# Kernel tuning notes

Measured on AMD Instinct MI355X. Metric: run time of the kernel, lower is better.

The kernel has to match this reference:

```python
import jax, jax.numpy as jnp
import numpy as np

N, L, D = 4096, 16, 768        # nodes, max name tokens, gpt2 embed dim
NH_NAME = 4                    # name-encoder attention heads
H, NH, NL, C = 1024, 8, 4, 16  # hidden, encoder heads, encoder layers, classes
XF = 256                       # raw node feature dim; feat_dim = XF + D = 1024
VOCAB = 50257


def _ln(x, g, b, eps=1e-5):
    m = jnp.mean(x, axis=-1, keepdims=True)
    v = jnp.var(x, axis=-1, keepdims=True)
    return (x - m) * jax.lax.rsqrt(v + eps) * g + b


def _mha(x, in_w, in_b, out_w, out_b, nh, key_mask=None):
    # x: [B, S, E]; in_w: [3E, E] (torch nn.MultiheadAttention packed qkv)
    B, S, E = x.shape
    dh = E // nh
    qkv = x @ in_w.T + in_b
    q, k, v = jnp.split(qkv, 3, axis=-1)
    q = q.reshape(B, S, nh, dh)
    k = k.reshape(B, S, nh, dh)
    v = v.reshape(B, S, nh, dh)
    scores = jnp.einsum('bqhd,bkhd->bhqk', q, k) / jnp.sqrt(jnp.asarray(dh, x.dtype))
    if key_mask is not None:
        scores = jnp.where(key_mask[:, None, None, :], scores, jnp.asarray(-1e9, x.dtype))
    a = jax.nn.softmax(scores, axis=-1)
    o = jnp.einsum('bhqk,bkhd->bqhd', a, v).reshape(B, S, E)
    return o @ out_w.T + out_b


def setup_inputs() -> dict:
    key = jax.random.key(0)
    ks = jax.random.split(key, 16)
    s = 0.02
    r = lambda i, shape: jax.random.normal(ks[i], shape, jnp.float32) * s
    return {
        'name_tokens': jax.random.randint(ks[0], (N, L), 0, VOCAB),
        'name_lens': jax.random.randint(ks[1], (N,), 1, L + 1),
        'x_feats': jax.random.normal(ks[2], (N, XF), jnp.float32),
        'wte': r(3, (VOCAB, D)),
        'mha_in_w': r(4, (3 * D, D)), 'mha_in_b': jnp.zeros((3 * D,), jnp.float32),
        'mha_out_w': r(5, (D, D)), 'mha_out_b': jnp.zeros((D,), jnp.float32),
        'bott_w': r(6, (H, XF + D)), 'bott_b': jnp.zeros((H,), jnp.float32),
        'enc_in_w': r(7, (NL, 3 * H, H)), 'enc_in_b': jnp.zeros((NL, 3 * H), jnp.float32),
        'enc_out_w': r(8, (NL, H, H)), 'enc_out_b': jnp.zeros((NL, H), jnp.float32),
        'enc_ln1_g': jnp.ones((NL, H), jnp.float32), 'enc_ln1_b': jnp.zeros((NL, H), jnp.float32),
        'enc_ln2_g': jnp.ones((NL, H), jnp.float32), 'enc_ln2_b': jnp.zeros((NL, H), jnp.float32),
        'enc_ff1_w': r(9, (NL, 2 * H, H)), 'enc_ff1_b': jnp.zeros((NL, 2 * H), jnp.float32),
        'enc_ff2_w': r(10, (NL, H, 2 * H)), 'enc_ff2_b': jnp.zeros((NL, H), jnp.float32),
        'cls_w': r(11, (C, H)), 'cls_b': jnp.zeros((C,), jnp.float32),
    }


def reference(name_tokens, name_lens, x_feats, wte,
              mha_in_w, mha_in_b, mha_out_w, mha_out_b,
              bott_w, bott_b,
              enc_in_w, enc_in_b, enc_out_w, enc_out_b,
              enc_ln1_g, enc_ln1_b, enc_ln2_g, enc_ln2_b,
              enc_ff1_w, enc_ff1_b, enc_ff2_w, enc_ff2_b,
              cls_w, cls_b):
    # --- GraphNameEncoder: batched over all N ragged name sequences ---
    mask = jnp.arange(L)[None, :] < name_lens[:, None]          # [N, L] valid-token mask
    emb = wte[name_tokens]                                      # [N, L, D]
    attn = _mha(emb, mha_in_w, mha_in_b, mha_out_w, mha_out_b, NH_NAME, key_mask=mask)
    name_emb = jnp.sum(jnp.where(mask[:, :, None], attn, 0.0), axis=1)  # [N, D]
    x = jnp.concatenate([x_feats, name_emb], axis=-1)           # [N, XF + D]
    # --- bottleneck ---
    x = x @ bott_w.T + bott_b                                   # [N, H]
    # --- TransformerEncoder on seq_len=1 (x.unsqueeze(1)), post-norm, relu ---
    h = x[:, None, :]                                           # [N, 1, H]
    for l in range(NL):
        a = _mha(h, enc_in_w[l], enc_in_b[l], enc_out_w[l], enc_out_b[l], NH)
        h = _ln(h + a, enc_ln1_g[l], enc_ln1_b[l])
        f = jax.nn.relu(h @ enc_ff1_w[l].T + enc_ff1_b[l]) @ enc_ff2_w[l].T + enc_ff2_b[l]
        h = _ln(h + f, enc_ln2_g[l], enc_ln2_b[l])
    out = h @ cls_w.T + cls_b                                   # [N, 1, C]
    return out[:, 0, :]                                         # squeeze -> [N, C]
```

## Files before the change

kernel.cpp:

```cpp
#include <hip/hip_runtime.h>

typedef unsigned short bf16_t;
typedef __attribute__((ext_vector_type(8))) __bf16 bf16x8;
typedef __attribute__((ext_vector_type(4))) float f32x4;

__device__ __forceinline__ float bf2f(unsigned v) { return __uint_as_float(v << 16); }
__device__ __forceinline__ bf16_t f2bf(float f) {
  unsigned u = __float_as_uint(f);
  return (bf16_t)((u + 0x7fffu + ((u >> 16) & 1u)) >> 16);
}
__device__ __forceinline__ unsigned pack2(float a, float b) {
  return (unsigned)f2bf(a) | ((unsigned)f2bf(b) << 16);
}

__global__ __launch_bounds__(256) void scan_lens(const int* __restrict__ lens,
                                                 int* __restrict__ offs,
                                                 int* __restrict__ Mact) {
  __shared__ int wsum[4];
  const int t = threadIdx.x;
  int v[16]; int s = 0;
#pragma unroll
  for (int i = 0; i < 16; i++) { v[i] = lens[t * 16 + i]; s += v[i]; }
  const int lane = t & 63, w = t >> 6;
  int x = s;
#pragma unroll
  for (int o = 1; o < 64; o <<= 1) {
    int y = __shfl_up(x, o);
    if (lane >= o) x += y;
  }
  if (lane == 63) wsum[w] = x;
  __syncthreads();
  int base = 0;
  for (int i = 0; i < w; i++) base += wsum[i];
  int run = base + x - s;
#pragma unroll
  for (int i = 0; i < 16; i++) { offs[t * 16 + i] = run; run += v[i]; }
  if (t == 255) Mact[0] = run;
}

__global__ void cvt_f32_bf16(const float* __restrict__ src, bf16_t* __restrict__ dst, long n4) {
  long i = (long)blockIdx.x * blockDim.x + threadIdx.x;
  if (i >= n4) return;
  float4 v = ((const float4*)src)[i];
  ((uint2*)dst)[i] = make_uint2(pack2(v.x, v.y), pack2(v.z, v.w));
}

__global__ void cvt_encv(const float* __restrict__ src, bf16_t* __restrict__ dst, long n4) {
  long i = (long)blockIdx.x * blockDim.x + threadIdx.x;
  if (i >= n4) return;
  const long per = (1024L * 1024L) / 4;
  long l = i / per, r = i % per;
  const float* s = src + l * 3 * 1024 * 1024 + 2 * 1024 * 1024 + r * 4;
  float4 v = *(const float4*)s;
  ((uint2*)dst)[i] = make_uint2(pack2(v.x, v.y), pack2(v.z, v.w));
}

__global__ void gather_emb_c(const int* __restrict__ tok, const int* __restrict__ lens,
                             const int* __restrict__ offs, const float* __restrict__ wte,
                             bf16_t* __restrict__ emb) {
  long i = (long)blockIdx.x * blockDim.x + threadIdx.x;
  if (i >= 65536L * 192L) return;
  long nl = i / 192; int cg = (int)(i % 192);
  int n = (int)(nl >> 4), l = (int)(nl & 15);
  if (l >= lens[n]) return;
  long ro = (long)offs[n] + l;
  int t = tok[nl];
  float4 v = *(const float4*)(wte + (long)t * 768 + cg * 4);
  ((uint2*)emb)[ro * 192 + cg] = make_uint2(pack2(v.x, v.y), pack2(v.z, v.w));
}

__global__ void xfeat_lenf(const float* __restrict__ xf, const int* __restrict__ lens,
                           bf16_t* __restrict__ x, float* __restrict__ lenf) {
  long i = (long)blockIdx.x * blockDim.x + threadIdx.x;
  if (i < 4096) lenf[i] = (float)lens[i];
  if (i >= 4096L * 64L) return;
  int row = (int)(i >> 6); int c4 = (int)(i & 63) * 4;
  float4 v = *(const float4*)(xf + (long)row * 256 + c4);
  *(uint2*)(x + (long)row * 1024 + c4) = make_uint2(pack2(v.x, v.y), pack2(v.z, v.w));
}

#define BM 128
#define BN 128
#define BK 32

__device__ __forceinline__ void async16(const void* g, void* l) {
  __builtin_amdgcn_global_load_lds((const __attribute__((address_space(1))) void*)g,
                                   (__attribute__((address_space(3))) void*)l, 16, 0, 0);
}

__global__ __launch_bounds__(256, 2) void gemm_bt(
    const bf16_t* __restrict__ A, const bf16_t* __restrict__ W,
    const float* __restrict__ bias, bf16_t* __restrict__ C,
    int K, int ldc, const int* __restrict__ Mp) {
  const int m0 = blockIdx.y * BM;
  if (m0 >= *Mp) return;
  __shared__ __attribute__((aligned(16))) bf16_t As[BM * BK];
  __shared__ __attribute__((aligned(16))) bf16_t Bs[BN * BK];
  const int t = threadIdx.x;
  const int n0 = blockIdx.x * BN;
  const int lane = t & 63;
  const int wr = t >> 7;
  const int wc = (t >> 6) & 1;
  const int quad = lane >> 4;
  const int r16 = lane & 15;

  f32x4 acc[4][4] = {};

  const int c0 = t, c1 = t + 256;
  const int row0 = c0 >> 2, kp0 = (c0 & 3) << 3;
  const int row1 = c1 >> 2, kp1 = (c1 & 3) << 3;
  bf16_t* lA0 = As + (size_t)(c0 & ~63) * 8;
  bf16_t* lA1 = As + (size_t)(c1 & ~63) * 8;
  bf16_t* lB0 = Bs + (size_t)(c0 & ~63) * 8;
  bf16_t* lB1 = Bs + (size_t)(c1 & ~63) * 8;
  const bf16_t* Ab = A + (size_t)m0 * K;
  const bf16_t* Wb = W + (size_t)n0 * K;

  for (int k0 = 0; k0 < K; k0 += BK) {
    __syncthreads();
    async16(Ab + (size_t)row0 * K + k0 + kp0, lA0);
    async16(Ab + (size_t)row1 * K + k0 + kp1, lA1);
    async16(Wb + (size_t)row0 * K + k0 + kp0, lB0);
    async16(Wb + (size_t)row1 * K + k0 + kp1, lB1);
    __syncthreads();
    bf16x8 af[4], bfr[4];
#pragma unroll
    for (int i = 0; i < 4; i++) {
      af[i]  = *(const bf16x8*)(As + (wr * 64 + i * 16 + r16) * BK + quad * 8);
      bfr[i] = *(const bf16x8*)(Bs + (wc * 64 + i * 16 + r16) * BK + quad * 8);
    }
#pragma unroll
    for (int i = 0; i < 4; i++)
#pragma unroll
      for (int j = 0; j < 4; j++)
        acc[i][j] = __builtin_amdgcn_mfma_f32_16x16x32_bf16(af[i], bfr[j], acc[i][j], 0, 0, 0);
  }

  const int colb = n0 + wc * 64;
  const int rowb = m0 + wr * 64;
#pragma unroll
  for (int j = 0; j < 4; j++) {
    int col = colb + j * 16 + r16;
    float bv = bias ? bias[col] : 0.0f;
#pragma unroll
    for (int i = 0; i < 4; i++) {
      int rbase = rowb + i * 16 + quad * 4;
#pragma unroll
      for (int r = 0; r < 4; r++) {
        int row = rbase + r;
        C[(size_t)row * ldc + col] = f2bf(acc[i][j][r] + bv);
      }
    }
  }
}

template <bool RELU>
__global__ __launch_bounds__(256, 4) void gemm64(
    const bf16_t* __restrict__ A, const bf16_t* __restrict__ W,
    const float* __restrict__ bias, const float* __restrict__ rowscale,
    bf16_t* __restrict__ C, int K, int ldc) {
  __shared__ __attribute__((aligned(16))) bf16_t As[64 * 64];
  __shared__ __attribute__((aligned(16))) bf16_t Bs[64 * 64];
  const int t = threadIdx.x;
  const int m0 = blockIdx.y * 64, n0 = blockIdx.x * 64;
  const int lane = t & 63, wr = t >> 7, wc = (t >> 6) & 1;
  const int quad = lane >> 4, r16 = lane & 15;
  f32x4 acc[2][2] = {};
  const int c0 = t, c1 = t + 256;
  const int row0 = c0 >> 3, kp0 = (((c0 & 7) ^ (row0 & 7)) << 3);
  const int row1 = c1 >> 3, kp1 = (((c1 & 7) ^ (row1 & 7)) << 3);
  bf16_t* lA0 = As + (size_t)(c0 & ~63) * 8;
  bf16_t* lA1 = As + (size_t)(c1 & ~63) * 8;
  bf16_t* lB0 = Bs + (size_t)(c0 & ~63) * 8;
  bf16_t* lB1 = Bs + (size_t)(c1 & ~63) * 8;
  const bf16_t* Ab = A + (size_t)m0 * K;
  const bf16_t* Wb = W + (size_t)n0 * K;

  for (int k0 = 0; k0 < K; k0 += 64) {
    __syncthreads();
    async16(Ab + (size_t)row0 * K + k0 + kp0, lA0);
    async16(Ab + (size_t)row1 * K + k0 + kp1, lA1);
    async16(Wb + (size_t)row0 * K + k0 + kp0, lB0);
    async16(Wb + (size_t)row1 * K + k0 + kp1, lB1);
    __syncthreads();
#pragma unroll
    for (int kk8 = 0; kk8 < 8; kk8 += 4) {
      bf16x8 af[2], bfr[2];
#pragma unroll
      for (int i = 0; i < 2; i++) {
        int Ra = wr * 32 + i * 16 + r16;
        af[i] = *(const bf16x8*)(As + Ra * 64 + (((kk8 + quad) ^ (Ra & 7)) << 3));
        int Rb = wc * 32 + i * 16 + r16;
        bfr[i] = *(const bf16x8*)(Bs + Rb * 64 + (((kk8 + quad) ^ (Rb & 7)) << 3));
      }
#pragma unroll
      for (int i = 0; i < 2; i++)
#pragma unroll
        for (int j = 0; j < 2; j++)
          acc[i][j] = __builtin_amdgcn_mfma_f32_16x16x32_bf16(af[i], bfr[j], acc[i][j], 0, 0, 0);
    }
  }

  const int colb = n0 + wc * 32, rowb = m0 + wr * 32;
#pragma unroll
  for (int j = 0; j < 2; j++) {
    int col = colb + j * 16 + r16;
    float bv = bias ? bias[col] : 0.0f;
#pragma unroll
    for (int i = 0; i < 2; i++) {
      int rbase = rowb + i * 16 + quad * 4;
#pragma unroll
      for (int r = 0; r < 4; r++) {
        int row = rbase + r;
        float sc = rowscale ? rowscale[row] : 1.0f;
        float v = acc[i][j][r] + bv * sc;
        if (RELU) v = fmaxf(v, 0.0f);
        C[(size_t)row * ldc + col] = f2bf(v);
      }
    }
  }
}

__global__ __launch_bounds__(64) void attn_name(const bf16_t* __restrict__ qkv,
                                                const int* __restrict__ lens,
                                                const int* __restrict__ offs,
                                                bf16_t* __restrict__ s) {
  const int n = blockIdx.x, h = blockIdx.y;
  const int lane = threadIdx.x;
  __shared__ unsigned short qs[16][208];
  __shared__ unsigned short ks[16][208];
  __shared__ unsigned short vs[16][208];
  __shared__ float ps[16][16];
  __shared__ float wj[16];
  const int len = lens[n];
  const bf16_t* base = qkv + (size_t)offs[n] * 2304 + h * 192;
  for (int g = lane; g < len * 48; g += 64) {
    int row = g / 48, c4 = (g % 48) * 4;
    const bf16_t* p = base + (size_t)row * 2304 + c4;
    uint2 a;
    a = *(const uint2*)p;
    *(unsigned*)&qs[row][c4] = a.x; *(unsigned*)&qs[row][c4 + 2] = a.y;
    a = *(const uint2*)(p + 768);
    *(unsigned*)&ks[row][c4] = a.x; *(unsigned*)&ks[row][c4 + 2] = a.y;
    a = *(const uint2*)(p + 1536);
    *(unsigned*)&vs[row][c4] = a.x; *(unsigned*)&vs[row][c4 + 2] = a.y;
  }
  __syncthreads();
  {
    const int l = lane >> 2, j0 = (lane & 3) * 4;
    float s0 = 0, s1 = 0, s2 = 0, s3 = 0;
    for (int d = 0; d < 192; d++) {
      float q = bf2f(qs[l][d]);
      s0 += q * bf2f(ks[j0 + 0][d]);
      s1 += q * bf2f(ks[j0 + 1][d]);
      s2 += q * bf2f(ks[j0 + 2][d]);
      s3 += q * bf2f(ks[j0 + 3][d]);
    }
    const float sc = 0.07216878f;
    ps[l][j0 + 0] = s0 * sc; ps[l][j0 + 1] = s1 * sc;
    ps[l][j0 + 2] = s2 * sc; ps[l][j0 + 3] = s3 * sc;
  }
  __syncthreads();
  if (lane < 16) {
    float m = -1e30f;
    for (int j = 0; j < len; j++) m = fmaxf(m, ps[lane][j]);
    float sum = 0.f;
    for (int j = 0; j < len; j++) sum += __expf(ps[lane][j] - m);
    float inv = 1.0f / sum;
    for (int j = 0; j < 16; j++) ps[lane][j] = (j < len) ? __expf(ps[lane][j] - m) * inv : 0.0f;
  }
  __syncthreads();
  if (lane < 16) {
    float a = 0.f;
    for (int l2 = 0; l2 < len; l2++) a += ps[l2][lane];
    wj[lane] = a;
  }
  __syncthreads();
  for (int d = lane; d < 192; d += 64) {
    float a = 0.f;
    for (int j = 0; j < len; j++) a += wj[j] * bf2f(vs[j][d]);
    s[(size_t)n * 768 + h * 192 + d] = f2bf(a);
  }
}

__global__ __launch_bounds__(256) void ln_res(bf16_t* __restrict__ h, const bf16_t* __restrict__ d,
                                              const float* __restrict__ g, const float* __restrict__ b) {
  const int n = blockIdx.x, t = threadIdx.x;
  __shared__ float s1[4], s2[4];
  bf16_t* hr = h + (size_t)n * 1024;
  const bf16_t* dr = d + (size_t)n * 1024;
  float x[4];
  float sum = 0.f, ss = 0.f;
#pragma unroll
  for (int i = 0; i < 4; i++) {
    int c = t + i * 256;
    float v = bf2f(hr[c]) + bf2f(dr[c]);
    x[i] = v; sum += v; ss += v * v;
  }
#pragma unroll
  for (int o = 32; o > 0; o >>= 1) { sum += __shfl_down(sum, o); ss += __shfl_down(ss, o); }
  if ((t & 63) == 0) { s1[t >> 6] = sum; s2[t >> 6] = ss; }
  __syncthreads();
  sum = s1[0] + s1[1] + s1[2] + s1[3];
  ss  = s2[0] + s2[1] + s2[2] + s2[3];
  const float mean = sum * (1.0f / 1024.0f);
  const float var = ss * (1.0f / 1024.0f) - mean * mean;
  const float rstd = rsqrtf(var + 1e-5f);
#pragma unroll
  for (int i = 0; i < 4; i++) {
    int c = t + i * 256;
    hr[c] = f2bf((x[i] - mean) * rstd * g[c] + b[c]);
  }
}

__global__ __launch_bounds__(256) void cls_head(const bf16_t* __restrict__ h,
                                                const float* __restrict__ cw,
                                                const float* __restrict__ cb,
                                                float* __restrict__ out) {
  const int n = blockIdx.x, t = threadIdx.x, wave = t >> 6, lane = t & 63;
  const bf16_t* hr = h + (size_t)n * 1024;
  for (int c = wave; c < 16; c += 4) {
    const float* wr = cw + c * 1024;
    float acc = 0.f;
    for (int i = lane; i < 1024; i += 64) acc += bf2f(hr[i]) * wr[i];
#pragma unroll
    for (int o = 32; o > 0; o >>= 1) acc += __shfl_down(acc, o);
    if (lane == 0) out[(size_t)n * 16 + c] = acc + cb[c];
  }
}

extern "C" void kernel_launch(void* const* d_in, const int* in_sizes, int n_in,
                              void* d_out, int out_size, void* d_ws, size_t ws_size,
                              hipStream_t stream) {
  (void)in_sizes; (void)n_in; (void)out_size; (void)ws_size;
  const int* name_tokens = (const int*)d_in[0];
  const int* name_lens   = (const int*)d_in[1];
  const float* x_feats   = (const float*)d_in[2];
  const float* wte       = (const float*)d_in[3];
  const float* mha_in_w  = (const float*)d_in[4];
  const float* mha_in_b  = (const float*)d_in[5];
  const float* mha_out_w = (const float*)d_in[6];
  const float* mha_out_b = (const float*)d_in[7];
  const float* bott_w    = (const float*)d_in[8];
  const float* bott_b    = (const float*)d_in[9];
  const float* enc_in_w  = (const float*)d_in[10];
  const float* enc_in_b  = (const float*)d_in[11];
  const float* enc_out_w = (const float*)d_in[12];
  const float* enc_out_b = (const float*)d_in[13];
  const float* enc_ln1_g = (const float*)d_in[14];
  const float* enc_ln1_b = (const float*)d_in[15];
  const float* enc_ln2_g = (const float*)d_in[16];
  const float* enc_ln2_b = (const float*)d_in[17];
  const float* enc_ff1_w = (const float*)d_in[18];
  const float* enc_ff1_b = (const float*)d_in[19];
  const float* enc_ff2_w = (const float*)d_in[20];
  const float* enc_ff2_b = (const float*)d_in[21];
  const float* cls_w     = (const float*)d_in[22];
  const float* cls_b     = (const float*)d_in[23];
  float* out = (float*)d_out;

  char* base = (char*)d_ws;
  size_t off = 0;
  auto alloc = [&](size_t bytes) -> char* {
    char* p = base + off;
    off = (off + bytes + 255) & ~(size_t)255;
    return p;
  };
  bf16_t* w_qkv  = (bf16_t*)alloc((size_t)2304 * 768 * 2);
  bf16_t* w_out  = (bf16_t*)alloc((size_t)768 * 768 * 2);
  bf16_t* w_bott = (bf16_t*)alloc((size_t)1024 * 1024 * 2);
  bf16_t* w_encv = (bf16_t*)alloc((size_t)4 * 1024 * 1024 * 2);
  bf16_t* w_enco = (bf16_t*)alloc((size_t)4 * 1024 * 1024 * 2);
  bf16_t* w_ff1  = (bf16_t*)alloc((size_t)4 * 2048 * 1024 * 2);
  bf16_t* w_ff2  = (bf16_t*)alloc((size_t)4 * 1024 * 2048 * 2);
  float*  lenf   = (float*)alloc((size_t)4096 * 4);
  int*    offs   = (int*)alloc((size_t)4096 * 4);
  int*    Mact   = (int*)alloc((size_t)256);
  char* reuse = alloc((size_t)65536 * 768 * 2);
  bf16_t* emb = (bf16_t*)reuse;
  bf16_t* s_  = (bf16_t*)reuse;
  bf16_t* x_  = (bf16_t*)(reuse + 6291456);
  bf16_t* h_  = (bf16_t*)(reuse + 6291456 + 8388608);
  bf16_t* v_  = (bf16_t*)(reuse + 6291456 + 2 * 8388608);
  bf16_t* a_  = (bf16_t*)(reuse + 6291456 + 3 * 8388608);
  bf16_t* f1_ = (bf16_t*)(reuse + 6291456 + 4 * 8388608);
  bf16_t* qkv = (bf16_t*)alloc((size_t)65536 * 2304 * 2);

  dim3 b256(256);
  auto g1 = [](long n4) { return dim3((unsigned)((n4 + 255) / 256)); };

  scan_lens<<<dim3(1), b256, 0, stream>>>(name_lens, offs, Mact);

  cvt_f32_bf16<<<g1(442368), b256, 0, stream>>>(mha_in_w, w_qkv, 442368L);
  cvt_f32_bf16<<<g1(147456), b256, 0, stream>>>(mha_out_w, w_out, 147456L);
  cvt_f32_bf16<<<g1(262144), b256, 0, stream>>>(bott_w, w_bott, 262144L);
  cvt_encv<<<g1(1048576), b256, 0, stream>>>(enc_in_w, w_encv, 1048576L);
  cvt_f32_bf16<<<g1(1048576), b256, 0, stream>>>(enc_out_w, w_enco, 1048576L);
  cvt_f32_bf16<<<g1(2097152), b256, 0, stream>>>(enc_ff1_w, w_ff1, 2097152L);
  cvt_f32_bf16<<<g1(2097152), b256, 0, stream>>>(enc_ff2_w, w_ff2, 2097152L);

  gather_emb_c<<<dim3(49152), b256, 0, stream>>>(name_tokens, name_lens, offs, wte, emb);
  gemm_bt<<<dim3(18, 512), b256, 0, stream>>>(emb, w_qkv, mha_in_b, qkv, 768, 2304, Mact);
  xfeat_lenf<<<dim3(1024), b256, 0, stream>>>(x_feats, name_lens, x_, lenf);
  attn_name<<<dim3(4096, 4), dim3(64), 0, stream>>>(qkv, name_lens, offs, s_);
  gemm64<false><<<dim3(12, 64), b256, 0, stream>>>(s_, w_out, mha_out_b, lenf,
                                                   x_ + 256, 768, 1024);
  gemm64<false><<<dim3(16, 64), b256, 0, stream>>>(x_, w_bott, bott_b, (const float*)nullptr,
                                                   h_, 1024, 1024);
  for (int l = 0; l < 4; l++) {
    gemm64<false><<<dim3(16, 64), b256, 0, stream>>>(
        h_, w_encv + (size_t)l * 1024 * 1024, enc_in_b + l * 3072 + 2048,
        (const float*)nullptr, v_, 1024, 1024);
    gemm64<false><<<dim3(16, 64), b256, 0, stream>>>(
        v_, w_enco + (size_t)l * 1024 * 1024, enc_out_b + l * 1024,
        (const float*)nullptr, a_, 1024, 1024);
    ln_res<<<dim3(4096), b256, 0, stream>>>(h_, a_, enc_ln1_g + l * 1024, enc_ln1_b + l * 1024);
    gemm64<true><<<dim3(32, 64), b256, 0, stream>>>(
        h_, w_ff1 + (size_t)l * 2048 * 1024, enc_ff1_b + l * 2048,
        (const float*)nullptr, f1_, 1024, 2048);
    gemm64<false><<<dim3(16, 64), b256, 0, stream>>>(
        f1_, w_ff2 + (size_t)l * 1024 * 2048, enc_ff2_b + l * 1024,
        (const float*)nullptr, v_, 2048, 1024);
    ln_res<<<dim3(4096), b256, 0, stream>>>(h_, v_, enc_ln2_g + l * 1024, enc_ln2_b + l * 1024);
  }
  cls_head<<<dim3(4096), b256, 0, stream>>>(h_, cls_w, cls_b, out);
}
```

Baseline: 1.224 ms.

## Fold V and output projections into one weight; retile GEMMs to 128x64; merge conversions

```diff
diff --git a/kernel.cpp b/kernel.cpp
--- a/kernel.cpp
+++ b/kernel.cpp
@@ -38,21 +38,64 @@
   if (t == 255) Mact[0] = run;
 }
 
-__global__ void cvt_f32_bf16(const float* __restrict__ src, bf16_t* __restrict__ dst, long n4) {
+__global__ void cvt_all(const float* __restrict__ mha_in_w, const float* __restrict__ mha_out_w,
+                        const float* __restrict__ bott_w, const float* __restrict__ enc_out_w,
+                        const float* __restrict__ enc_ff1_w, const float* __restrict__ enc_ff2_w,
+                        bf16_t* __restrict__ w_qkv, bf16_t* __restrict__ w_out,
+                        bf16_t* __restrict__ w_bott, bf16_t* __restrict__ w_enco,
+                        bf16_t* __restrict__ w_ff1, bf16_t* __restrict__ w_ff2) {
   long i = (long)blockIdx.x * blockDim.x + threadIdx.x;
-  if (i >= n4) return;
-  float4 v = ((const float4*)src)[i];
-  ((uint2*)dst)[i] = make_uint2(pack2(v.x, v.y), pack2(v.z, v.w));
-}
-
-__global__ void cvt_encv(const float* __restrict__ src, bf16_t* __restrict__ dst, long n4) {
-  long i = (long)blockIdx.x * blockDim.x + threadIdx.x;
-  if (i >= n4) return;
-  const long per = (1024L * 1024L) / 4;
-  long l = i / per, r = i % per;
-  const float* s = src + l * 3 * 1024 * 1024 + 2 * 1024 * 1024 + r * 4;
-  float4 v = *(const float4*)s;
-  ((uint2*)dst)[i] = make_uint2(pack2(v.x, v.y), pack2(v.z, v.w));
+  const float* src; bf16_t* dst; long j;
+  if (i < 442368L)        { src = mha_in_w;  dst = w_qkv;  j = i; }
+  else if (i < 589824L)   { src = mha_out_w; dst = w_out;  j = i - 442368L; }
+  else if (i < 851968L)   { src = bott_w;    dst = w_bott; j = i - 589824L; }
+  else if (i < 1900544L)  { src = enc_out_w; dst = w_enco; j = i - 851968L; }
+  else if (i < 3997696L)  { src = enc_ff1_w; dst = w_ff1;  j = i - 1900544L; }
+  else if (i < 6094848L)  { src = enc_ff2_w; dst = w_ff2;  j = i - 3997696L; }
+  else return;
+  float4 v = ((const float4*)src)[j];
+  ((uint2*)dst)[j] = make_uint2(pack2(v.x, v.y), pack2(v.z, v.w));
+}
+
+__global__ __launch_bounds__(256) void cvt_encvT(const float* __restrict__ enc_in_w,
+                                                 bf16_t* __restrict__ dst) {
+  __shared__ float lt[64][65];
+  const int t = threadIdx.x;
+  const int tx = t & 15, ty = t >> 4;
+  const int n0 = blockIdx.x * 64, k0 = blockIdx.y * 64, l = blockIdx.z;
+  const float* src = enc_in_w + (size_t)l * 3 * 1024 * 1024 + 2 * 1024 * 1024;
+#pragma unroll
+  for (int p = 0; p < 4; p++) {
+    int kr = p * 16 + ty;
+    float4 v = *(const float4*)(src + (size_t)(k0 + kr) * 1024 + n0 + tx * 4);
+    lt[kr][tx * 4 + 0] = v.x; lt[kr][tx * 4 + 1] = v.y;
+    lt[kr][tx * 4 + 2] = v.z; lt[kr][tx * 4 + 3] = v.w;
+  }
+  __syncthreads();
+  bf16_t* d = dst + (size_t)l * 1024 * 1024;
+#pragma unroll
+  for (int p = 0; p < 4; p++) {
+    int nr = p * 16 + ty;
+    float a = lt[tx * 4 + 0][nr], b = lt[tx * 4 + 1][nr];
+    float c = lt[tx * 4 + 2][nr], e = lt[tx * 4 + 3][nr];
+    *(uint2*)(d + (size_t)(n0 + nr) * 1024 + k0 + tx * 4) = make_uint2(pack2(a, b), pack2(c, e));
+  }
+}
+
+__global__ __launch_bounds__(256) void bias_vo(const float* __restrict__ enc_out_w,
+                                               const float* __restrict__ enc_in_b,
+                                               const float* __restrict__ enc_out_b,
+                                               float* __restrict__ b_vo) {
+  const int t = threadIdx.x, lane = t & 63, w = t >> 6;
+  const int m = blockIdx.x * 4 + w, l = blockIdx.y;
+  const float* wr = enc_out_w + (size_t)l * 1024 * 1024 + (size_t)m * 1024;
+  const float* bv = enc_in_b + l * 3072 + 2048;
+  float acc = 0.f;
+#pragma unroll
+  for (int i = 0; i < 16; i++) acc += wr[lane + i * 64] * bv[lane + i * 64];
+#pragma unroll
+  for (int o = 32; o > 0; o >>= 1) acc += __shfl_down(acc, o);
+  if (lane == 0) b_vo[l * 1024 + m] = acc + enc_out_b[l * 1024 + m];
 }
 
 __global__ void gather_emb_c(const int* __restrict__ tok, const int* __restrict__ lens,
@@ -79,10 +122,6 @@
   *(uint2*)(x + (long)row * 1024 + c4) = make_uint2(pack2(v.x, v.y), pack2(v.z, v.w));
 }
 
-#define BM 128
-#define BN 128
-#define BK 32
-
 __device__ __forceinline__ void async16(const void* g, void* l) {
   __builtin_amdgcn_global_load_lds((const __attribute__((address_space(1))) void*)g,
                                    (__attribute__((address_space(3))) void*)l, 16, 0, 0);
@@ -92,17 +131,15 @@
     const bf16_t* __restrict__ A, const bf16_t* __restrict__ W,
     const float* __restrict__ bias, bf16_t* __restrict__ C,
     int K, int ldc, const int* __restrict__ Mp) {
-  const int m0 = blockIdx.y * BM;
+  const int m0 = blockIdx.y * 128;
   if (m0 >= *Mp) return;
-  __shared__ __attribute__((aligned(16))) bf16_t As[BM * BK];
-  __shared__ __attribute__((aligned(16))) bf16_t Bs[BN * BK];
+  __shared__ __attribute__((aligned(16))) bf16_t As[128 * 32];
+  __shared__ __attribute__((aligned(16))) bf16_t Bs[128 * 32];
   const int t = threadIdx.x;
-  const int n0 = blockIdx.x * BN;
+  const int n0 = blockIdx.x * 128;
   const int lane = t & 63;
-  const int wr = t >> 7;
-  const int wc = (t >> 6) & 1;
-  const int quad = lane >> 4;
-  const int r16 = lane & 15;
+  const int wr = t >> 7, wc = (t >> 6) & 1;
+  const int quad = lane >> 4, r16 = lane & 15;
 
   f32x4 acc[4][4] = {};
 
@@ -116,7 +153,7 @@
   const bf16_t* Ab = A + (size_t)m0 * K;
   const bf16_t* Wb = W + (size_t)n0 * K;
 
-  for (int k0 = 0; k0 < K; k0 += BK) {
+  for (int k0 = 0; k0 < K; k0 += 32) {
     __syncthreads();
     async16(Ab + (size_t)row0 * K + k0 + kp0, lA0);
     async16(Ab + (size_t)row1 * K + k0 + kp1, lA1);
@@ -126,8 +163,8 @@
     bf16x8 af[4], bfr[4];
 #pragma unroll
     for (int i = 0; i < 4; i++) {
-      af[i]  = *(const bf16x8*)(As + (wr * 64 + i * 16 + r16) * BK + quad * 8);
-      bfr[i] = *(const bf16x8*)(Bs + (wc * 64 + i * 16 + r16) * BK + quad * 8);
+      af[i]  = *(const bf16x8*)(As + (wr * 64 + i * 16 + r16) * 32 + quad * 8);
+      bfr[i] = *(const bf16x8*)(Bs + (wc * 64 + i * 16 + r16) * 32 + quad * 8);
     }
 #pragma unroll
     for (int i = 0; i < 4; i++)
@@ -136,8 +173,7 @@
         acc[i][j] = __builtin_amdgcn_mfma_f32_16x16x32_bf16(af[i], bfr[j], acc[i][j], 0, 0, 0);
   }
 
-  const int colb = n0 + wc * 64;
-  const int rowb = m0 + wr * 64;
+  const int colb = n0 + wc * 64, rowb = m0 + wr * 64;
 #pragma unroll
   for (int j = 0; j < 4; j++) {
     int col = colb + j * 16 + r16;
@@ -155,59 +191,59 @@
 }
 
 template <bool RELU>
-__global__ __launch_bounds__(256, 4) void gemm64(
+__global__ __launch_bounds__(256, 4) void gemm_bn(
     const bf16_t* __restrict__ A, const bf16_t* __restrict__ W,
     const float* __restrict__ bias, const float* __restrict__ rowscale,
-    bf16_t* __restrict__ C, int K, int ldc) {
-  __shared__ __attribute__((aligned(16))) bf16_t As[64 * 64];
-  __shared__ __attribute__((aligned(16))) bf16_t Bs[64 * 64];
+    bf16_t* __restrict__ C, int K, int ldc, long sA, long sW, long sC) {
+  __shared__ __attribute__((aligned(16))) bf16_t As[128 * 32];
+  __shared__ __attribute__((aligned(16))) bf16_t Bs[64 * 32];
+  const int z = blockIdx.z;
+  A += (size_t)z * sA; W += (size_t)z * sW; C += (size_t)z * sC;
   const int t = threadIdx.x;
-  const int m0 = blockIdx.y * 64, n0 = blockIdx.x * 64;
-  const int lane = t & 63, wr = t >> 7, wc = (t >> 6) & 1;
+  const int m0 = blockIdx.y * 128, n0 = blockIdx.x * 64;
+  const int lane = t & 63;
+  const int wr = t >> 7, wc = (t >> 6) & 1;
   const int quad = lane >> 4, r16 = lane & 15;
-  f32x4 acc[2][2] = {};
+
+  f32x4 acc[4][2] = {};
+
   const int c0 = t, c1 = t + 256;
-  const int row0 = c0 >> 3, kp0 = (((c0 & 7) ^ (row0 & 7)) << 3);
-  const int row1 = c1 >> 3, kp1 = (((c1 & 7) ^ (row1 & 7)) << 3);
+  const int rowA0 = c0 >> 2, kpA0 = (c0 & 3) << 3;
+  const int rowA1 = c1 >> 2, kpA1 = (c1 & 3) << 3;
+  const int rowB = t >> 2, kpB = (t & 3) << 3;
   bf16_t* lA0 = As + (size_t)(c0 & ~63) * 8;
   bf16_t* lA1 = As + (size_t)(c1 & ~63) * 8;
-  bf16_t* lB0 = Bs + (size_t)(c0 & ~63) * 8;
-  bf16_t* lB1 = Bs + (size_t)(c1 & ~63) * 8;
+  bf16_t* lB  = Bs + (size_t)(t & ~63) * 8;
   const bf16_t* Ab = A + (size_t)m0 * K;
   const bf16_t* Wb = W + (size_t)n0 * K;
 
-  for (int k0 = 0; k0 < K; k0 += 64) {
+  for (int k0 = 0; k0 < K; k0 += 32) {
     __syncthreads();
-    async16(Ab + (size_t)row0 * K + k0 + kp0, lA0);
-    async16(Ab + (size_t)row1 * K + k0 + kp1, lA1);
-    async16(Wb + (size_t)row0 * K + k0 + kp0, lB0);
-    async16(Wb + (size_t)row1 * K + k0 + kp1, lB1);
+    async16(Ab + (size_t)rowA0 * K + k0 + kpA0, lA0);
+    async16(Ab + (size_t)rowA1 * K + k0 + kpA1, lA1);
+    async16(Wb + (size_t)rowB * K + k0 + kpB, lB);
     __syncthreads();
-#pragma unroll
-    for (int kk8 = 0; kk8 < 8; kk8 += 4) {
-      bf16x8 af[2], bfr[2];
-#pragma unroll
-      for (int i = 0; i < 2; i++) {
-        int Ra = wr * 32 + i * 16 + r16;
-        af[i] = *(const bf16x8*)(As + Ra * 64 + (((kk8 + quad) ^ (Ra & 7)) << 3));
-        int Rb = wc * 32 + i * 16 + r16;
-        bfr[i] = *(const bf16x8*)(Bs + Rb * 64 + (((kk8 + quad) ^ (Rb & 7)) << 3));
-      }
-#pragma unroll
-      for (int i = 0; i < 2; i++)
-#pragma unroll
-        for (int j = 0; j < 2; j++)
-          acc[i][j] = __builtin_amdgcn_mfma_f32_16x16x32_bf16(af[i], bfr[j], acc[i][j], 0, 0, 0);
-    }
-  }
-
-  const int colb = n0 + wc * 32, rowb = m0 + wr * 32;
+    bf16x8 af[4], bfr[2];
+#pragma unroll
+    for (int i = 0; i < 4; i++)
+      af[i] = *(const bf16x8*)(As + (wr * 64 + i * 16 + r16) * 32 + quad * 8);
+#pragma unroll
+    for (int j = 0; j < 2; j++)
+      bfr[j] = *(const bf16x8*)(Bs + (wc * 32 + j * 16 + r16) * 32 + quad * 8);
+#pragma unroll
+    for (int i = 0; i < 4; i++)
+#pragma unroll
+      for (int j = 0; j < 2; j++)
+        acc[i][j] = __builtin_amdgcn_mfma_f32_16x16x32_bf16(af[i], bfr[j], acc[i][j], 0, 0, 0);
+  }
+
+  const int colb = n0 + wc * 32, rowb = m0 + wr * 64;
 #pragma unroll
   for (int j = 0; j < 2; j++) {
     int col = colb + j * 16 + r16;
     float bv = bias ? bias[col] : 0.0f;
 #pragma unroll
-    for (int i = 0; i < 2; i++) {
+    for (int i = 0; i < 4; i++) {
       int rbase = rowb + i * 16 + quad * 4;
 #pragma unroll
       for (int r = 0; r < 4; r++) {
@@ -366,16 +402,18 @@
     off = (off + bytes + 255) & ~(size_t)255;
     return p;
   };
-  bf16_t* w_qkv  = (bf16_t*)alloc((size_t)2304 * 768 * 2);
-  bf16_t* w_out  = (bf16_t*)alloc((size_t)768 * 768 * 2);
-  bf16_t* w_bott = (bf16_t*)alloc((size_t)1024 * 1024 * 2);
-  bf16_t* w_encv = (bf16_t*)alloc((size_t)4 * 1024 * 1024 * 2);
-  bf16_t* w_enco = (bf16_t*)alloc((size_t)4 * 1024 * 1024 * 2);
-  bf16_t* w_ff1  = (bf16_t*)alloc((size_t)4 * 2048 * 1024 * 2);
-  bf16_t* w_ff2  = (bf16_t*)alloc((size_t)4 * 1024 * 2048 * 2);
-  float*  lenf   = (float*)alloc((size_t)4096 * 4);
-  int*    offs   = (int*)alloc((size_t)4096 * 4);
-  int*    Mact   = (int*)alloc((size_t)256);
+  bf16_t* w_qkv   = (bf16_t*)alloc((size_t)2304 * 768 * 2);
+  bf16_t* w_out   = (bf16_t*)alloc((size_t)768 * 768 * 2);
+  bf16_t* w_bott  = (bf16_t*)alloc((size_t)1024 * 1024 * 2);
+  bf16_t* w_enco  = (bf16_t*)alloc((size_t)4 * 1024 * 1024 * 2);
+  bf16_t* w_encvT = (bf16_t*)alloc((size_t)4 * 1024 * 1024 * 2);
+  bf16_t* w_vo    = (bf16_t*)alloc((size_t)4 * 1024 * 1024 * 2);
+  bf16_t* w_ff1   = (bf16_t*)alloc((size_t)4 * 2048 * 1024 * 2);
+  bf16_t* w_ff2   = (bf16_t*)alloc((size_t)4 * 1024 * 2048 * 2);
+  float*  b_vo    = (float*)alloc((size_t)4 * 1024 * 4);
+  float*  lenf    = (float*)alloc((size_t)4096 * 4);
+  int*    offs    = (int*)alloc((size_t)4096 * 4);
+  int*    Mact    = (int*)alloc((size_t)256);
   char* reuse = alloc((size_t)65536 * 768 * 2);
   bf16_t* emb = (bf16_t*)reuse;
   bf16_t* s_  = (bf16_t*)reuse;
@@ -387,40 +425,37 @@
   bf16_t* qkv = (bf16_t*)alloc((size_t)65536 * 2304 * 2);
 
   dim3 b256(256);
-  auto g1 = [](long n4) { return dim3((unsigned)((n4 + 255) / 256)); };
+  const float* nof = nullptr;
 
   scan_lens<<<dim3(1), b256, 0, stream>>>(name_lens, offs, Mact);
-
-  cvt_f32_bf16<<<g1(442368), b256, 0, stream>>>(mha_in_w, w_qkv, 442368L);
-  cvt_f32_bf16<<<g1(147456), b256, 0, stream>>>(mha_out_w, w_out, 147456L);
-  cvt_f32_bf16<<<g1(262144), b256, 0, stream>>>(bott_w, w_bott, 262144L);
-  cvt_encv<<<g1(1048576), b256, 0, stream>>>(enc_in_w, w_encv, 1048576L);
-  cvt_f32_bf16<<<g1(1048576), b256, 0, stream>>>(enc_out_w, w_enco, 1048576L);
-  cvt_f32_bf16<<<g1(2097152), b256, 0, stream>>>(enc_ff1_w, w_ff1, 2097152L);
-  cvt_f32_bf16<<<g1(2097152), b256, 0, stream>>>(enc_ff2_w, w_ff2, 2097152L);
+  cvt_all<<<dim3(23808), b256, 0, stream>>>(mha_in_w, mha_out_w, bott_w, enc_out_w,
+                                            enc_ff1_w, enc_ff2_w,
+                                            w_qkv, w_out, w_bott, w_enco, w_ff1, w_ff2);
+  cvt_encvT<<<dim3(16, 16, 4), b256, 0, stream>>>(enc_in_w, w_encvT);
+  bias_vo<<<dim3(256, 4), b256, 0, stream>>>(enc_out_w, enc_in_b, enc_out_b, b_vo);
 
   gather_emb_c<<<dim3(49152), b256, 0, stream>>>(name_tokens, name_lens, offs, wte, emb);
   gemm_bt<<<dim3(18, 512), b256, 0, stream>>>(emb, w_qkv, mha_in_b, qkv, 768, 2304, Mact);
   xfeat_lenf<<<dim3(1024), b256, 0, stream>>>(x_feats, name_lens, x_, lenf);
   attn_name<<<dim3(4096, 4), dim3(64), 0, stream>>>(qkv, name_lens, offs, s_);
-  gemm64<false><<<dim3(12, 64), b256, 0, stream>>>(s_, w_out, mha_out_b, lenf,
-                                                   x_ + 256, 768, 1024);
-  gemm64<false><<<dim3(16, 64), b256, 0, stream>>>(x_, w_bott, bott_b, (const float*)nullptr,
-                                                   h_, 1024, 1024);
+
+  gemm_bn<false><<<dim3(16, 8, 4), b256, 0, stream>>>(
+      w_enco, w_encvT, nof, nof, w_vo, 1024, 1024,
+      1024L * 1024, 1024L * 1024, 1024L * 1024);
+
+  gemm_bn<false><<<dim3(12, 32, 1), b256, 0, stream>>>(
+      s_, w_out, mha_out_b, lenf, x_ + 256, 768, 1024, 0, 0, 0);
+  gemm_bn<false><<<dim3(16, 32, 1), b256, 0, stream>>>(
+      x_, w_bott, bott_b, nof, h_, 1024, 1024, 0, 0, 0);
+
   for (int l = 0; l < 4; l++) {
-    gemm64<false><<<dim3(16, 64), b256, 0, stream>>>(
-        h_, w_encv + (size_t)l * 1024 * 1024, enc_in_b + l * 3072 + 2048,
-        (const float*)nullptr, v_, 1024, 1024);
-    gemm64<false><<<dim3(16, 64), b256, 0, stream>>>(
-        v_, w_enco + (size_t)l * 1024 * 1024, enc_out_b + l * 1024,
-        (const float*)nullptr, a_, 1024, 1024);
+    gemm_bn<false><<<dim3(16, 32, 1), b256, 0, stream>>>(
+        h_, w_vo + (size_t)l * 1024 * 1024, b_vo + l * 1024, nof, a_, 1024, 1024, 0, 0, 0);
     ln_res<<<dim3(4096), b256, 0, stream>>>(h_, a_, enc_ln1_g + l * 1024, enc_ln1_b + l * 1024);
-    gemm64<true><<<dim3(32, 64), b256, 0, stream>>>(
-        h_, w_ff1 + (size_t)l * 2048 * 1024, enc_ff1_b + l * 2048,
-        (const float*)nullptr, f1_, 1024, 2048);
-    gemm64<false><<<dim3(16, 64), b256, 0, stream>>>(
-        f1_, w_ff2 + (size_t)l * 1024 * 2048, enc_ff2_b + l * 1024,
-        (const float*)nullptr, v_, 2048, 1024);
+    gemm_bn<true><<<dim3(32, 32, 1), b256, 0, stream>>>(
+        h_, w_ff1 + (size_t)l * 2048 * 1024, enc_ff1_b + l * 2048, nof, f1_, 1024, 2048, 0, 0, 0);
+    gemm_bn<false><<<dim3(16, 32, 1), b256, 0, stream>>>(
+        f1_, w_ff2 + (size_t)l * 1024 * 2048, enc_ff2_b + l * 1024, nof, v_, 2048, 1024, 0, 0, 0);
     ln_res<<<dim3(4096), b256, 0, stream>>>(h_, v_, enc_ln2_g + l * 1024, enc_ln2_b + l * 1024);
   }
   cls_head<<<dim3(4096), b256, 0, stream>>>(h_, cls_w, cls_b, out);
```

Result: slower. 1.278 ms (+4.5%).
